# Performance work log

Hardware: AMD Instinct MI355X
Metric: run time of the kernel (lower is better)

## Reference

```python
import jax, jax.numpy as jnp
import numpy as np

BETA = 10.0  # fixed buffer: torch.ones(1, num_centers) * 10


def setup_inputs() -> dict:
    key = jax.random.key(0)
    k1, k2, k3 = jax.random.split(key, 3)
    n, M, d, n_out = 65536, 1024, 64, 3
    x = jax.random.normal(k1, (n, d), dtype=jnp.float32)
    centers = jax.random.normal(k2, (M, d), dtype=jnp.float32)
    # nn.Linear init in the module: weight ~ N(0, 0.02), bias = 0
    W = jax.random.normal(k3, (n_out, M + d), dtype=jnp.float32) * 0.02
    b = jnp.zeros((n_out,), dtype=jnp.float32)
    return {"x": x, "centers": centers, "W": W, "b": b}


def reference(x, centers, W, b):
    x2 = jnp.sum(x * x, axis=1, keepdims=True)          # [n, 1]
    c2 = jnp.sum(centers * centers, axis=1)             # [M]
    d2 = x2 + c2[None, :] - 2.0 * (x @ centers.T)       # [n, M]
    rbf = jnp.exp(-BETA * d2)                           # Gaussian RBF
    feat = jnp.concatenate([x, rbf], axis=1)            # [n, d + M]
    return feat @ W.T + b                               # [n, n_out]
```

## Files before the change

### kernel.cpp

```cpp
#include <hip/hip_runtime.h>
#include <math.h>

typedef short bf16x8 __attribute__((ext_vector_type(8)));
typedef float f32x4 __attribute__((ext_vector_type(4)));
typedef unsigned int uint32;

#define BETA 10.0f
#define THRESH -80.0f

#define C_OFF   0
#define C2_OFF  131072
#define XB_OFF  135168
#define W_OFF   151552
#define X2_OFF  152320
#define RED_OFF 152832
#define LDS_TOT 154368

__device__ __forceinline__ uint32 f2bf_rtne(float f) {
    uint32 u = __float_as_uint(f);
    u += 0x7FFFu + ((u >> 16) & 1u);
    return u >> 16;
}
__device__ __forceinline__ uint32 pk_rtne(float a, float b) {
    return f2bf_rtne(a) | (f2bf_rtne(b) << 16);
}
__device__ __forceinline__ float bf2f(short s) {
    return __uint_as_float(((uint32)(unsigned short)s) << 16);
}
__device__ __forceinline__ f32x4 vmax4(f32x4 a, f32x4 b) {
    f32x4 r;
    r[0] = fmaxf(a[0], b[0]); r[1] = fmaxf(a[1], b[1]);
    r[2] = fmaxf(a[2], b[2]); r[3] = fmaxf(a[3], b[3]);
    return r;
}

#define GLDS(g, l) __builtin_amdgcn_global_load_lds( \
    (const __attribute__((address_space(1))) unsigned int*)(g), \
    (__attribute__((address_space(3))) unsigned int*)(l), 16, 0, 0)

__global__ void rbfn_prep(const float* __restrict__ centers,
                          uint32* __restrict__ cbf,
                          float* __restrict__ c2m) {
    const int tid = threadIdx.x;
    const int j = blockIdx.x * 64 + (tid >> 2);
    const int seg = tid & 3;
    const float4* cp = (const float4*)(centers + j * 64 + seg * 16);
    const float4 f0 = cp[0], f1 = cp[1], f2 = cp[2], f3 = cp[3];
    float s = f0.x*f0.x + f0.y*f0.y + f0.z*f0.z + f0.w*f0.w
            + f1.x*f1.x + f1.y*f1.y + f1.z*f1.z + f1.w*f1.w
            + f2.x*f2.x + f2.y*f2.y + f2.z*f2.z + f2.w*f2.w
            + f3.x*f3.x + f3.y*f3.y + f3.z*f3.z + f3.w*f3.w;
    uint4 p0, p1;
    p0.x = pk_rtne(f0.x, f0.y); p0.y = pk_rtne(f0.z, f0.w);
    p0.z = pk_rtne(f1.x, f1.y); p0.w = pk_rtne(f1.z, f1.w);
    p1.x = pk_rtne(f2.x, f2.y); p1.y = pk_rtne(f2.z, f2.w);
    p1.z = pk_rtne(f3.x, f3.y); p1.w = pk_rtne(f3.z, f3.w);
    char* base = (char*)cbf + (j >> 4) * 2048 + (j & 15) * 16;
    *(uint4*)(base + (seg * 2 + 0) * 256) = p0;
    *(uint4*)(base + (seg * 2 + 1) * 256) = p1;
    s += __shfl_xor(s, 1);
    s += __shfl_xor(s, 2);
    if (seg == 0) c2m[j] = -BETA * s;
}

__global__ __launch_bounds__(512, 2) void rbfn_main(
    const float* __restrict__ x,
    const char* __restrict__ ws,
    const float* __restrict__ W,
    const float* __restrict__ bias,
    const float* __restrict__ centers,
    float* __restrict__ out)
{
    __shared__ __align__(16) char lds[LDS_TOT];

    const int tid = threadIdx.x;
    const int wv = tid >> 6;
    const int lane = tid & 63;
    const int quad = lane >> 4;
    const int l15 = lane & 15;
    const int row0 = blockIdx.x * 128;

    const float bb0 = bias[0], bb1 = bias[1], bb2 = bias[2];

    {
        const char* g = ws + wv * 1024 + lane * 16;
        char* l = lds + wv * 1024;
        #pragma unroll
        for (int it = 0; it < 16; ++it)
            GLDS(g + it * 8192, l + it * 8192);
        if (wv < 4)
            GLDS(ws + 131072 + wv * 1024 + lane * 16, lds + 131072 + wv * 1024);
    }

    {
        const float4* xg = (const float4*)(x + (size_t)row0 * 64);
        #pragma unroll
        for (int i = 0; i < 4; ++i) {
            const int f = tid + 512 * i;
            const float4 v = xg[f];
            const int row = f >> 4, sg = f & 15;
            uint2 q;
            q.x = pk_rtne(v.x, v.y);
            q.y = pk_rtne(v.z, v.w);
            *(uint2*)(lds + XB_OFF + (row >> 4) * 2048 + (sg >> 1) * 256 +
                      (row & 15) * 16 + (sg & 1) * 8) = q;
        }
    }
    if (tid < 48) {
        const int k = tid >> 4, c = tid & 15;
        *((float4*)(lds + W_OFF) + tid) = *((const float4*)(W + k * 1088) + c);
    }

    __syncthreads();

    bf16x8 af[8][2];
    #pragma unroll
    for (int rt = 0; rt < 8; ++rt) {
        const char* ab = lds + XB_OFF + rt * 2048 + l15 * 16;
        af[rt][0] = *(const bf16x8*)(ab + quad * 256);
        af[rt][1] = *(const bf16x8*)(ab + (4 + quad) * 256);
    }

    {
        const int r = tid >> 2, qq = tid & 3;
        const char* xr = lds + XB_OFF + (r >> 4) * 2048 + (r & 15) * 16;
        const bf16x8 h0 = *(const bf16x8*)(xr + (qq * 2 + 0) * 256);
        const bf16x8 h1 = *(const bf16x8*)(xr + (qq * 2 + 1) * 256);
        const float* w0 = (const float*)(lds + W_OFF) + 0 * 64 + qq * 16;
        const float* w1 = (const float*)(lds + W_OFF) + 1 * 64 + qq * 16;
        const float* w2 = (const float*)(lds + W_OFF) + 2 * 64 + qq * 16;
        float s2 = 0.f, d0 = 0.f, d1 = 0.f, d2 = 0.f;
        #pragma unroll
        for (int e = 0; e < 8; ++e) {
            const float a = bf2f(h0[e]), b = bf2f(h1[e]);
            s2 = fmaf(a, a, s2); s2 = fmaf(b, b, s2);
            d0 = fmaf(a, w0[e], d0); d0 = fmaf(b, w0[8 + e], d0);
            d1 = fmaf(a, w1[e], d1); d1 = fmaf(b, w1[8 + e], d1);
            d2 = fmaf(a, w2[e], d2); d2 = fmaf(b, w2[8 + e], d2);
        }
        #pragma unroll
        for (int m = 1; m <= 2; m <<= 1) {
            s2 += __shfl_xor(s2, m);
            d0 += __shfl_xor(d0, m);
            d1 += __shfl_xor(d1, m);
            d2 += __shfl_xor(d2, m);
        }
        if (qq == 0) {
            ((float*)(lds + X2_OFF))[r] = s2;
            float* red = (float*)(lds + RED_OFF);
            red[r * 3 + 0] = d0 + bb0;
            red[r * 3 + 1] = d1 + bb1;
            red[r * 3 + 2] = d2 + bb2;
        }
    }
    __syncthreads();

    const float* px2 = (const float*)(lds + X2_OFF);
    float mn = 1e30f;
    #pragma unroll
    for (int rt = 0; rt < 8; ++rt) {
        const float4 q4 = *(const float4*)(px2 + rt * 16 + quad * 4);
        mn = fminf(mn, fminf(fminf(q4.x, q4.y), fminf(q4.z, q4.w)));
    }
    const float prermax = -BETA * mn;

    const char* cB = lds + wv * 16384 + quad * 256 + l15 * 16;
    const float* c2p = (const float*)(lds + C2_OFF) + wv * 128 + l15;
    float gm = -1e30f;
    #pragma unroll
    for (int ct = 0; ct < 8; ++ct) {
        const bf16x8 b0 = *(const bf16x8*)(cB + ct * 2048);
        const bf16x8 b1 = *(const bf16x8*)(cB + ct * 2048 + 1024);
        const float c2v = c2p[ct * 16];
        f32x4 acc[8];
        #pragma unroll
        for (int rt = 0; rt < 8; ++rt) {
            const f32x4 z = {0.f, 0.f, 0.f, 0.f};
            acc[rt] = __builtin_amdgcn_mfma_f32_16x16x32_bf16(af[rt][0], b0, z, 0, 0, 0);
            acc[rt] = __builtin_amdgcn_mfma_f32_16x16x32_bf16(af[rt][1], b1, acc[rt], 0, 0, 0);
        }
        f32x4 m0 = vmax4(vmax4(acc[0], acc[1]), vmax4(acc[2], acc[3]));
        f32x4 m1 = vmax4(vmax4(acc[4], acc[5]), vmax4(acc[6], acc[7]));
        m0 = vmax4(m0, m1);
        const float m = fmaxf(fmaxf(m0[0], m0[1]), fmaxf(m0[2], m0[3]));
        gm = fmaxf(gm, fmaf(2.0f * BETA, m, c2v));
    }
    const float bound = gm + prermax;

    if (__builtin_expect(__ballot(bound > THRESH) != 0ull, 0)) {
        float* red = (float*)(lds + RED_OFF);
        #pragma clang loop unroll(disable)
        for (int ct = 0; ct < 8; ++ct) {
            const int j = wv * 128 + ct * 16 + l15;
            #pragma clang loop unroll(disable)
            for (int rr = 0; rr < 32; ++rr) {
                const int r = (rr >> 2) * 16 + quad * 4 + (rr & 3);
                const float* xr = x + (size_t)(row0 + r) * 64;
                const float* cr = centers + (size_t)j * 64;
                float d2 = 0.f;
                #pragma clang loop unroll(disable)
                for (int k = 0; k < 64; ++k) {
                    const float df = xr[k] - cr[k];
                    d2 = fmaf(df, df, d2);
                }
                const float arg = -BETA * d2;
                if (arg > -87.f) {
                    const float e = expf(arg);
                    atomicAdd(&red[r * 3 + 0], e * W[0 * 1088 + 64 + j]);
                    atomicAdd(&red[r * 3 + 1], e * W[1 * 1088 + 64 + j]);
                    atomicAdd(&red[r * 3 + 2], e * W[2 * 1088 + 64 + j]);
                }
            }
        }
    }
    __syncthreads();

    if (tid < 96)
        ((float4*)out)[blockIdx.x * 96 + tid] = *((const float4*)(lds + RED_OFF) + tid);
}

extern "C" void kernel_launch(void* const* d_in, const int* in_sizes, int n_in,
                              void* d_out, int out_size, void* d_ws, size_t ws_size,
                              hipStream_t stream) {
    const float* x       = (const float*)d_in[0];
    const float* centers = (const float*)d_in[1];
    const float* W       = (const float*)d_in[2];
    const float* b       = (const float*)d_in[3];
    float* out = (float*)d_out;

    uint32* cbf = (uint32*)d_ws;
    float*  c2m = (float*)((char*)d_ws + 131072);

    const int n = in_sizes[0] / 64;

    rbfn_prep<<<16, 256, 0, stream>>>(centers, cbf, c2m);
    rbfn_main<<<n / 128, 512, 0, stream>>>(x, (const char*)d_ws, W, b, centers, out);
}
```

Before: 80.09 us.

## Process two row tiles per block to reuse LDS-resident centers

Each block now handles 256 rows as two 128-row tiles, so the 128KB bf16 centers block staged in LDS is loaded once and reused for both tiles. The grid is halved to match. The x data for the second tile is prefetched into registers up front and packed into LDS after the first tile's barrier, overlapping its global load with the first tile's work. This cuts redundant L2-to-LDS center traffic, at the cost of fewer blocks, a longer serial chain per block and more registers.

```diff
diff --git a/kernel.cpp b/kernel.cpp
--- a/kernel.cpp
+++ b/kernel.cpp
@@ -8,13 +8,13 @@
 #define BETA 10.0f
 #define THRESH -80.0f
 
-#define C_OFF   0
-#define C2_OFF  131072
-#define XB_OFF  135168
-#define W_OFF   151552
-#define X2_OFF  152320
-#define RED_OFF 152832
-#define LDS_TOT 154368
+#define C_OFF    0
+#define C2_OFF   131072
+#define XB_OFF   135168
+#define W_OFF    151552
+#define X2_OFF   152320
+#define RED_OFF  152832
+#define LDS_TOT  155904
 
 __device__ __forceinline__ uint32 f2bf_rtne(float f) {
     uint32 u = __float_as_uint(f);
@@ -78,7 +78,7 @@
     const int lane = tid & 63;
     const int quad = lane >> 4;
     const int l15 = lane & 15;
-    const int row0 = blockIdx.x * 128;
+    const int row0 = blockIdx.x * 256;
 
     const float bb0 = bias[0], bb1 = bias[1], bb2 = bias[2];
 
@@ -92,131 +92,150 @@
             GLDS(ws + 131072 + wv * 1024 + lane * 16, lds + 131072 + wv * 1024);
     }
 
+    float4 xv[2][4];
     {
         const float4* xg = (const float4*)(x + (size_t)row0 * 64);
         #pragma unroll
-        for (int i = 0; i < 4; ++i) {
-            const int f = tid + 512 * i;
-            const float4 v = xg[f];
-            const int row = f >> 4, sg = f & 15;
-            uint2 q;
-            q.x = pk_rtne(v.x, v.y);
-            q.y = pk_rtne(v.z, v.w);
-            *(uint2*)(lds + XB_OFF + (row >> 4) * 2048 + (sg >> 1) * 256 +
-                      (row & 15) * 16 + (sg & 1) * 8) = q;
-        }
+        for (int i = 0; i < 4; ++i) xv[0][i] = xg[tid + 512 * i];
+        #pragma unroll
+        for (int i = 0; i < 4; ++i) xv[1][i] = xg[2048 + tid + 512 * i];
     }
     if (tid < 48) {
         const int k = tid >> 4, c = tid & 15;
         *((float4*)(lds + W_OFF) + tid) = *((const float4*)(W + k * 1088) + c);
     }
+    #pragma unroll
+    for (int i = 0; i < 4; ++i) {
+        const int f = tid + 512 * i;
+        const float4 v = xv[0][i];
+        const int row = f >> 4, sg = f & 15;
+        uint2 q; q.x = pk_rtne(v.x, v.y); q.y = pk_rtne(v.z, v.w);
+        *(uint2*)(lds + XB_OFF + (row >> 4) * 2048 + (sg >> 1) * 256 +
+                  (row & 15) * 16 + (sg & 1) * 8) = q;
+    }
 
     __syncthreads();
 
     bf16x8 af[8][2];
-    #pragma unroll
-    for (int rt = 0; rt < 8; ++rt) {
-        const char* ab = lds + XB_OFF + rt * 2048 + l15 * 16;
-        af[rt][0] = *(const bf16x8*)(ab + quad * 256);
-        af[rt][1] = *(const bf16x8*)(ab + (4 + quad) * 256);
-    }
-
-    {
-        const int r = tid >> 2, qq = tid & 3;
-        const char* xr = lds + XB_OFF + (r >> 4) * 2048 + (r & 15) * 16;
-        const bf16x8 h0 = *(const bf16x8*)(xr + (qq * 2 + 0) * 256);
-        const bf16x8 h1 = *(const bf16x8*)(xr + (qq * 2 + 1) * 256);
-        const float* w0 = (const float*)(lds + W_OFF) + 0 * 64 + qq * 16;
-        const float* w1 = (const float*)(lds + W_OFF) + 1 * 64 + qq * 16;
-        const float* w2 = (const float*)(lds + W_OFF) + 2 * 64 + qq * 16;
-        float s2 = 0.f, d0 = 0.f, d1 = 0.f, d2 = 0.f;
-        #pragma unroll
-        for (int e = 0; e < 8; ++e) {
-            const float a = bf2f(h0[e]), b = bf2f(h1[e]);
-            s2 = fmaf(a, a, s2); s2 = fmaf(b, b, s2);
-            d0 = fmaf(a, w0[e], d0); d0 = fmaf(b, w0[8 + e], d0);
-            d1 = fmaf(a, w1[e], d1); d1 = fmaf(b, w1[8 + e], d1);
-            d2 = fmaf(a, w2[e], d2); d2 = fmaf(b, w2[8 + e], d2);
-        }
-        #pragma unroll
-        for (int m = 1; m <= 2; m <<= 1) {
-            s2 += __shfl_xor(s2, m);
-            d0 += __shfl_xor(d0, m);
-            d1 += __shfl_xor(d1, m);
-            d2 += __shfl_xor(d2, m);
-        }
-        if (qq == 0) {
-            ((float*)(lds + X2_OFF))[r] = s2;
-            float* red = (float*)(lds + RED_OFF);
-            red[r * 3 + 0] = d0 + bb0;
-            red[r * 3 + 1] = d1 + bb1;
-            red[r * 3 + 2] = d2 + bb2;
-        }
-    }
-    __syncthreads();
-
-    const float* px2 = (const float*)(lds + X2_OFF);
-    float mn = 1e30f;
-    #pragma unroll
-    for (int rt = 0; rt < 8; ++rt) {
-        const float4 q4 = *(const float4*)(px2 + rt * 16 + quad * 4);
-        mn = fminf(mn, fminf(fminf(q4.x, q4.y), fminf(q4.z, q4.w)));
-    }
-    const float prermax = -BETA * mn;
-
     const char* cB = lds + wv * 16384 + quad * 256 + l15 * 16;
     const float* c2p = (const float*)(lds + C2_OFF) + wv * 128 + l15;
-    float gm = -1e30f;
+
     #pragma unroll
-    for (int ct = 0; ct < 8; ++ct) {
-        const bf16x8 b0 = *(const bf16x8*)(cB + ct * 2048);
-        const bf16x8 b1 = *(const bf16x8*)(cB + ct * 2048 + 1024);
-        const float c2v = c2p[ct * 16];
-        f32x4 acc[8];
+    for (int t = 0; t < 2; ++t) {
         #pragma unroll
         for (int rt = 0; rt < 8; ++rt) {
-            const f32x4 z = {0.f, 0.f, 0.f, 0.f};
-            acc[rt] = __builtin_amdgcn_mfma_f32_16x16x32_bf16(af[rt][0], b0, z, 0, 0, 0);
-            acc[rt] = __builtin_amdgcn_mfma_f32_16x16x32_bf16(af[rt][1], b1, acc[rt], 0, 0, 0);
-        }
-        f32x4 m0 = vmax4(vmax4(acc[0], acc[1]), vmax4(acc[2], acc[3]));
-        f32x4 m1 = vmax4(vmax4(acc[4], acc[5]), vmax4(acc[6], acc[7]));
-        m0 = vmax4(m0, m1);
-        const float m = fmaxf(fmaxf(m0[0], m0[1]), fmaxf(m0[2], m0[3]));
-        gm = fmaxf(gm, fmaf(2.0f * BETA, m, c2v));
-    }
-    const float bound = gm + prermax;
-
-    if (__builtin_expect(__ballot(bound > THRESH) != 0ull, 0)) {
-        float* red = (float*)(lds + RED_OFF);
-        #pragma clang loop unroll(disable)
+            const char* ab = lds + XB_OFF + rt * 2048 + l15 * 16;
+            af[rt][0] = *(const bf16x8*)(ab + quad * 256);
+            af[rt][1] = *(const bf16x8*)(ab + (4 + quad) * 256);
+        }
+        {
+            const int r = tid >> 2, qq = tid & 3;
+            const char* xr = lds + XB_OFF + (r >> 4) * 2048 + (r & 15) * 16;
+            const bf16x8 h0 = *(const bf16x8*)(xr + (qq * 2 + 0) * 256);
+            const bf16x8 h1 = *(const bf16x8*)(xr + (qq * 2 + 1) * 256);
+            const float* w0 = (const float*)(lds + W_OFF) + 0 * 64 + qq * 16;
+            const float* w1 = (const float*)(lds + W_OFF) + 1 * 64 + qq * 16;
+            const float* w2 = (const float*)(lds + W_OFF) + 2 * 64 + qq * 16;
+            float s2 = 0.f, d0 = 0.f, d1 = 0.f, d2 = 0.f;
+            #pragma unroll
+            for (int e = 0; e < 8; ++e) {
+                const float a = bf2f(h0[e]), b = bf2f(h1[e]);
+                s2 = fmaf(a, a, s2); s2 = fmaf(b, b, s2);
+                d0 = fmaf(a, w0[e], d0); d0 = fmaf(b, w0[8 + e], d0);
+                d1 = fmaf(a, w1[e], d1); d1 = fmaf(b, w1[8 + e], d1);
+                d2 = fmaf(a, w2[e], d2); d2 = fmaf(b, w2[8 + e], d2);
+            }
+            #pragma unroll
+            for (int m = 1; m <= 2; m <<= 1) {
+                s2 += __shfl_xor(s2, m);
+                d0 += __shfl_xor(d0, m);
+                d1 += __shfl_xor(d1, m);
+                d2 += __shfl_xor(d2, m);
+            }
+            if (qq == 0) {
+                ((float*)(lds + X2_OFF))[r] = s2;
+                float* red = (float*)(lds + RED_OFF + t * 1536);
+                red[r * 3 + 0] = d0 + bb0;
+                red[r * 3 + 1] = d1 + bb1;
+                red[r * 3 + 2] = d2 + bb2;
+            }
+        }
+        __syncthreads();
+
+        if (t == 0) {
+            #pragma unroll
+            for (int i = 0; i < 4; ++i) {
+                const int f = tid + 512 * i;
+                const float4 v = xv[1][i];
+                const int row = f >> 4, sg = f & 15;
+                uint2 q; q.x = pk_rtne(v.x, v.y); q.y = pk_rtne(v.z, v.w);
+                *(uint2*)(lds + XB_OFF + (row >> 4) * 2048 + (sg >> 1) * 256 +
+                          (row & 15) * 16 + (sg & 1) * 8) = q;
+            }
+        }
+
+        const float* px2 = (const float*)(lds + X2_OFF);
+        float mn = 1e30f;
+        #pragma unroll
+        for (int rt = 0; rt < 8; ++rt) {
+            const float4 q4 = *(const float4*)(px2 + rt * 16 + quad * 4);
+            mn = fminf(mn, fminf(fminf(q4.x, q4.y), fminf(q4.z, q4.w)));
+        }
+        const float prermax = -BETA * mn;
+
+        float gm = -1e30f;
+        #pragma unroll
         for (int ct = 0; ct < 8; ++ct) {
-            const int j = wv * 128 + ct * 16 + l15;
+            const bf16x8 b0 = *(const bf16x8*)(cB + ct * 2048);
+            const bf16x8 b1 = *(const bf16x8*)(cB + ct * 2048 + 1024);
+            const float c2v = c2p[ct * 16];
+            f32x4 acc[8];
+            #pragma unroll
+            for (int rt = 0; rt < 8; ++rt) {
+                const f32x4 z = {0.f, 0.f, 0.f, 0.f};
+                acc[rt] = __builtin_amdgcn_mfma_f32_16x16x32_bf16(af[rt][0], b0, z, 0, 0, 0);
+                acc[rt] = __builtin_amdgcn_mfma_f32_16x16x32_bf16(af[rt][1], b1, acc[rt], 0, 0, 0);
+            }
+            f32x4 m0 = vmax4(vmax4(acc[0], acc[1]), vmax4(acc[2], acc[3]));
+            f32x4 m1 = vmax4(vmax4(acc[4], acc[5]), vmax4(acc[6], acc[7]));
+            m0 = vmax4(m0, m1);
+            const float m = fmaxf(fmaxf(m0[0], m0[1]), fmaxf(m0[2], m0[3]));
+            gm = fmaxf(gm, fmaf(2.0f * BETA, m, c2v));
+        }
+        const float bound = gm + prermax;
+
+        if (__builtin_expect(__ballot(bound > THRESH) != 0ull, 0)) {
+            float* red = (float*)(lds + RED_OFF + t * 1536);
             #pragma clang loop unroll(disable)
-            for (int rr = 0; rr < 32; ++rr) {
-                const int r = (rr >> 2) * 16 + quad * 4 + (rr & 3);
-                const float* xr = x + (size_t)(row0 + r) * 64;
-                const float* cr = centers + (size_t)j * 64;
-                float d2 = 0.f;
+            for (int ct = 0; ct < 8; ++ct) {
+                const int j = wv * 128 + ct * 16 + l15;
                 #pragma clang loop unroll(disable)
-                for (int k = 0; k < 64; ++k) {
-                    const float df = xr[k] - cr[k];
-                    d2 = fmaf(df, df, d2);
+                for (int rr = 0; rr < 32; ++rr) {
+                    const int r = (rr >> 2) * 16 + quad * 4 + (rr & 3);
+                    const float* xr = x + (size_t)(row0 + t * 128 + r) * 64;
+                    const float* cr = centers + (size_t)j * 64;
+                    float d2 = 0.f;
+                    #pragma clang loop unroll(disable)
+                    for (int k = 0; k < 64; ++k) {
+                        const float df = xr[k] - cr[k];
+                        d2 = fmaf(df, df, d2);
+                    }
+                    const float arg = -BETA * d2;
+                    if (arg > -87.f) {
+                        const float e = expf(arg);
+                        atomicAdd(&red[r * 3 + 0], e * W[0 * 1088 + 64 + j]);
+                        atomicAdd(&red[r * 3 + 1], e * W[1 * 1088 + 64 + j]);
+                        atomicAdd(&red[r * 3 + 2], e * W[2 * 1088 + 64 + j]);
+                    }
                 }
-                const float arg = -BETA * d2;
-                if (arg > -87.f) {
-                    const float e = expf(arg);
-                    atomicAdd(&red[r * 3 + 0], e * W[0 * 1088 + 64 + j]);
-                    atomicAdd(&red[r * 3 + 1], e * W[1 * 1088 + 64 + j]);
-                    atomicAdd(&red[r * 3 + 2], e * W[2 * 1088 + 64 + j]);
-                }
-            }
-        }
-    }
-    __syncthreads();
-
-    if (tid < 96)
-        ((float4*)out)[blockIdx.x * 96 + tid] = *((const float4*)(lds + RED_OFF) + tid);
+            }
+        }
+        __syncthreads();
+
+        if (tid < 96)
+            ((float4*)out)[blockIdx.x * 192 + t * 96 + tid] =
+                *((const float4*)(lds + RED_OFF + t * 1536) + tid);
+    }
 }
 
 extern "C" void kernel_launch(void* const* d_in, const int* in_sizes, int n_in,
@@ -234,5 +253,5 @@
     const int n = in_sizes[0] / 64;
 
     rbfn_prep<<<16, 256, 0, stream>>>(centers, cbf, c2m);
-    rbfn_main<<<n / 128, 512, 0, stream>>>(x, (const char*)d_ws, W, b, centers, out);
-}
+    rbfn_main<<<n / 256, 512, 0, stream>>>(x, (const char*)d_ws, W, b, centers, out);
+}
```

Result: no change. 79.32 us (-1.0%).
